# Kernel tuning notes

Measured on AMD Instinct MI355X. Metric: run time of the kernel, lower is better.

## Reference

```python
import jax, jax.numpy as jnp
import numpy as np

B, C, E, S, L, N = 2, 256, 256, 3, 5, 128
HMAX = 128
LEVEL_SIZES = np.array([128, 64, 32, 16, 8])
STRIDES = np.array([8.0, 16.0, 32.0, 64.0, 128.0])
GROUPS = 8
EPS = 1e-5


def setup_inputs() -> dict:
    key = jax.random.key(0)
    ks = jax.random.split(key, 16)
    # Padded FPN pyramid stacked as [L, B, C, HMAX, HMAX]; level l valid in [:sz, :sz]
    fm = jnp.zeros((L, B, C, HMAX, HMAX), jnp.float32)
    for l in range(L):
        sz = int(LEVEL_SIZES[l])
        fm = fm.at[l, :, :, :sz, :sz].set(jax.random.normal(ks[l], (B, C, sz, sz), jnp.float32))
    # Boxes in 1024x1024 image coordinates (x1, y1, x2, y2)
    cxy = jax.random.uniform(ks[5], (N, 2), minval=60.0, maxval=960.0)
    wh = jax.random.uniform(ks[6], (N, 2), minval=8.0, maxval=96.0)
    boxes = jnp.concatenate([cxy - wh / 2, cxy + wh / 2], axis=1)
    batch_idx = jax.random.randint(ks[7], (N,), 0, B, jnp.int32)
    level_idx = jax.random.randint(ks[8], (N,), 0, L, jnp.int32)
    sym_ids = jax.random.randint(ks[9], (N,), 0, 6, jnp.int32)
    conv_w = jax.random.normal(ks[10], (E, C, 3, 3), jnp.float32) / np.float32(np.sqrt(C * 9))
    gn_scale = jnp.ones((E,), jnp.float32)
    gn_bias = jnp.zeros((E,), jnp.float32)
    head_w = jax.random.normal(ks[11], (E, E), jnp.float32) / np.float32(np.sqrt(E))
    head_b = jnp.zeros((E,), jnp.float32)
    spat_w = jax.random.normal(ks[12], (E, 4), jnp.float32) * 0.01
    spat_b = jnp.zeros((E,), jnp.float32)
    sym_emb = jax.random.normal(ks[13], (6, E), jnp.float32) * 0.05
    fuse_w = jax.random.normal(ks[14], (6, E, E), jnp.float32) / np.float32(np.sqrt(E))
    fuse_b = jnp.zeros((6, E), jnp.float32)
    return dict(feature_maps=fm, boxes=boxes, conv_w=conv_w, gn_scale=gn_scale,
                gn_bias=gn_bias, head_w=head_w, head_b=head_b, spat_w=spat_w,
                spat_b=spat_b, sym_emb=sym_emb, fuse_w=fuse_w, fuse_b=fuse_b,
                batch_idx=batch_idx, level_idx=level_idx, sym_ids=sym_ids)


def _roi_align(fm, boxes, batch_idx, level_idx):
    # Batched roi_align (aligned=False, sampling_ratio=1) over all boxes at once.
    scale = (1.0 / jnp.asarray(STRIDES, fm.dtype))[level_idx]          # [N]
    hv = jnp.asarray(LEVEL_SIZES, fm.dtype)[level_idx]                 # [N] valid H=W per box
    x1 = boxes[:, 0] * scale; y1 = boxes[:, 1] * scale
    x2 = boxes[:, 2] * scale; y2 = boxes[:, 3] * scale
    roi_w = jnp.maximum(x2 - x1, 1.0)
    roi_h = jnp.maximum(y2 - y1, 1.0)
    off = (jnp.arange(S, dtype=fm.dtype) + 0.5) / S                    # bin centers
    xs = x1[:, None] + off[None, :] * roi_w[:, None]                   # [N,S]
    ys = y1[:, None] + off[None, :] * roi_h[:, None]                   # [N,S]
    y = jnp.broadcast_to(ys[:, :, None], (ys.shape[0], S, S))          # [N,S,S]
    x = jnp.broadcast_to(xs[:, None, :], (xs.shape[0], S, S))
    hvb = hv[:, None, None]
    valid = (y > -1.0) & (y < hvb) & (x > -1.0) & (x < hvb)
    yc = jnp.clip(y, 0.0, hvb - 1.0)
    xc = jnp.clip(x, 0.0, hvb - 1.0)
    y0 = jnp.floor(yc).astype(jnp.int32)
    x0 = jnp.floor(xc).astype(jnp.int32)
    hi = (hvb - 1.0).astype(jnp.int32)
    y1i = jnp.minimum(y0 + 1, hi)
    x1i = jnp.minimum(x0 + 1, hi)
    ly = yc - y0.astype(fm.dtype)
    lx = xc - x0.astype(fm.dtype)
    lvl = level_idx[:, None, None]
    bix = batch_idx[:, None, None]

    def g(yi, xi):
        # gather only the 4 corner pixels -> [N,S,S,C]
        return fm[lvl, bix, :, yi, xi]

    v = ((1 - ly) * (1 - lx))[..., None] * g(y0, x0) \
      + ((1 - ly) * lx)[..., None] * g(y0, x1i) \
      + (ly * (1 - lx))[..., None] * g(y1i, x0) \
      + (ly * lx)[..., None] * g(y1i, x1i)
    v = jnp.where(valid[..., None], v, 0.0)
    return jnp.transpose(v, (0, 3, 1, 2))                              # [N,C,S,S]


def _forward(feature_maps, boxes, conv_w, gn_scale, gn_bias, head_w, head_b,
             spat_w, spat_b, sym_emb, fuse_w, fuse_b, batch_idx, level_idx, sym_ids):
    roi = _roi_align(feature_maps, boxes, batch_idx, level_idx)        # [N,C,S,S]
    h = jax.lax.conv_general_dilated(roi, conv_w, (1, 1), ((1, 1), (1, 1)),
                                     dimension_numbers=('NCHW', 'OIHW', 'NCHW'))  # [N,E,S,S]
    n = h.shape[0]
    hg = h.reshape(n, GROUPS, -1)
    mu = hg.mean(-1, keepdims=True)
    var = hg.var(-1, keepdims=True)
    hg = (hg - mu) * jax.lax.rsqrt(var + EPS)
    h = hg.reshape(h.shape) * gn_scale[None, :, None, None] + gn_bias[None, :, None, None]
    h = jax.nn.relu(h)
    h = h.reshape(n, E, -1).mean(-1)                                   # spatial mean -> [N,E]
    head_out = jax.nn.relu(h @ head_w.T + head_b)                      # sym_feat_nn + ReLU
    spat = jax.nn.relu(boxes @ spat_w.T + spat_b)                      # spatial_embeddings
    fused_in = head_out + spat + sym_emb[sym_ids]                      # + class embedding
    out = jax.nn.relu(jnp.einsum('ne,nfe->nf', fused_in, fuse_w[sym_ids]) + fuse_b[sym_ids])
    return out                                                          # [N,E]


def reference(feature_maps, boxes, conv_w, gn_scale, gn_bias, head_w, head_b,
              spat_w, spat_b, sym_emb, fuse_w, fuse_b, batch_idx, level_idx, sym_ids):
    return _forward(feature_maps, boxes, conv_w, gn_scale, gn_bias, head_w, head_b,
                    spat_w, spat_b, sym_emb, fuse_w, fuse_b, batch_idx, level_idx, sym_ids)
```

## Files before the change

kernel.cpp:

```cpp
#include <hip/hip_runtime.h>
#include <hip/hip_bf16.h>


__device__ __forceinline__ float bf_lo(unsigned u) { return __uint_as_float(u << 16); }
__device__ __forceinline__ float bf_hi(unsigned u) { return __uint_as_float(u & 0xffff0000u); }
__device__ __forceinline__ unsigned short f2bf(float f) {
    __hip_bfloat16 h = __float2bfloat16(f);
    return *(unsigned short*)&h;
}

__global__ __launch_bounds__(256) void prep_k(
    const float* __restrict__ conv_w,
    const float* __restrict__ head_w, const float* __restrict__ fuse_w,
    const float* __restrict__ fm, const float* __restrict__ boxes,
    const int* __restrict__ batch_idx, const int* __restrict__ level_idx,
    unsigned short* __restrict__ w8, unsigned short* __restrict__ w9,
    float* __restrict__ head_wT, float* __restrict__ fuse_wT,
    float* __restrict__ roiT) {
    int blk = blockIdx.x;
    int t = threadIdx.x;

    if (blk < 256) {
        int c = blk, e = t;
        const float* src = conv_w + ((size_t)e * 256 + c) * 9;
        unsigned short tmp[8];
#pragma unroll
        for (int k = 0; k < 8; ++k) tmp[k] = f2bf(src[k]);
        ((uint4*)w8)[(size_t)c * 256 + e] = *(const uint4*)tmp;
        w9[(size_t)c * 256 + e] = f2bf(src[8]);
        return;
    }

    if (blk < 704) {
        __shared__ float tile[32][33];
        int q = blk - 256;
        int z = q >> 6;
        int rem = q & 63;
        int bx = (rem & 7) * 32, by = (rem >> 3) * 32;
        const float* in = (z == 0) ? head_w : fuse_w + (size_t)(z - 1) * 65536;
        float* out = (z == 0) ? head_wT : fuse_wT + (size_t)(z - 1) * 65536;
        int tx = t & 31, ty = t >> 5;
#pragma unroll
        for (int i = 0; i < 32; i += 8)
            tile[ty + i][tx] = in[(size_t)(by + ty + i) * 256 + bx + tx];
        __syncthreads();
#pragma unroll
        for (int i = 0; i < 32; i += 8)
            out[(size_t)(bx + ty + i) * 256 + by + tx] = tile[tx][ty + i];
        return;
    }

    {
        int q = blk - 704;
        int n = q / 9, p = q % 9;
        int i = p / 3, j = p % 3;
        int c = t;

        int lvl = level_idx[n];
        int b = batch_idx[n];
        const float sizes[5]  = {128.f, 64.f, 32.f, 16.f, 8.f};
        const float invstr[5] = {1.f/8.f, 1.f/16.f, 1.f/32.f, 1.f/64.f, 1.f/128.f};
        float scale = invstr[lvl];
        float hv = sizes[lvl];

        float x1 = boxes[n*4+0] * scale, y1 = boxes[n*4+1] * scale;
        float x2 = boxes[n*4+2] * scale, y2 = boxes[n*4+3] * scale;
        float rw = fmaxf(x2 - x1, 1.f), rh = fmaxf(y2 - y1, 1.f);
        float x = x1 + (((float)j + 0.5f) / 3.f) * rw;
        float y = y1 + (((float)i + 0.5f) / 3.f) * rh;

        bool valid = (y > -1.f) && (y < hv) && (x > -1.f) && (x < hv);
        float yc = fminf(fmaxf(y, 0.f), hv - 1.f);
        float xc = fminf(fmaxf(x, 0.f), hv - 1.f);
        int y0 = (int)floorf(yc), x0 = (int)floorf(xc);
        int hi = (int)(hv - 1.f);
        int y1i = min(y0 + 1, hi), x1i = min(x0 + 1, hi);
        float ly = yc - (float)y0, lx = xc - (float)x0;

        const float* base = fm + (((size_t)lvl * 2 + b) * 256 + c) * (128 * 128);
        float v00 = base[y0 * 128 + x0];
        float v01 = base[y0 * 128 + x1i];
        float v10 = base[y1i * 128 + x0];
        float v11 = base[y1i * 128 + x1i];
        float v = (1.f - ly) * (1.f - lx) * v00 + (1.f - ly) * lx * v01 +
                  ly * (1.f - lx) * v10 + ly * lx * v11;
        roiT[((size_t)n * 9 + p) * 256 + c] = valid ? v : 0.f;
    }
}

__global__ __launch_bounds__(512, 2) void conv_gn_pool(
    const float* __restrict__ roiT,
    const unsigned short* __restrict__ w8, const unsigned short* __restrict__ w9,
    const float* __restrict__ gn_scale, const float* __restrict__ gn_bias,
    float* __restrict__ pooled) {
    __shared__ float lds_roi[256 * 12];
    __shared__ float red[4 * 64 * 9];

    int n  = blockIdx.x >> 2;
    int eq = blockIdx.x & 3;
    int t = threadIdx.x;
    int e_loc = t & 63;
    int ch = t >> 6;
    int e = eq * 64 + e_loc;

    const float* rsrc = roiT + (size_t)n * 2304;
    for (int v = t; v < 2304; v += 512) {
        int p = v >> 8, c = v & 255;
        lds_roi[c * 12 + p] = rsrc[v];
    }
    __syncthreads();

    float acc[9];
#pragma unroll
    for (int p = 0; p < 9; ++p) acc[p] = 0.f;

    int c0 = ch * 32;
    for (int c = c0; c < c0 + 32; ++c) {
        float r[9];
#pragma unroll
        for (int jj = 0; jj < 9; ++jj) r[jj] = lds_roi[c * 12 + jj];
        uint4 wa = ((const uint4*)w8)[(size_t)c * 256 + e];
        unsigned short w9v = w9[(size_t)c * 256 + e];
        float wv[9];
        wv[0] = bf_lo(wa.x); wv[1] = bf_hi(wa.x);
        wv[2] = bf_lo(wa.y); wv[3] = bf_hi(wa.y);
        wv[4] = bf_lo(wa.z); wv[5] = bf_hi(wa.z);
        wv[6] = bf_lo(wa.w); wv[7] = bf_hi(wa.w);
        wv[8] = bf_lo((unsigned)w9v);
#pragma unroll
        for (int ky = 0; ky < 3; ++ky) {
#pragma unroll
            for (int kx = 0; kx < 3; ++kx) {
                float w = wv[ky * 3 + kx];
#pragma unroll
                for (int oy = 0; oy < 3; ++oy) {
                    int iy = oy + ky - 1;
                    if (iy < 0 || iy > 2) continue;
#pragma unroll
                    for (int ox = 0; ox < 3; ++ox) {
                        int ix = ox + kx - 1;
                        if (ix < 0 || ix > 2) continue;
                        acc[oy * 3 + ox] = fmaf(w, r[iy * 3 + ix], acc[oy * 3 + ox]);
                    }
                }
            }
        }
    }

    if (ch >= 4) {
#pragma unroll
        for (int p = 0; p < 9; ++p) red[((ch - 4) * 64 + e_loc) * 9 + p] = acc[p];
    }
    __syncthreads();
    if (ch < 4) {
#pragma unroll
        for (int p = 0; p < 9; ++p) acc[p] += red[(ch * 64 + e_loc) * 9 + p];
    }
    __syncthreads();
    if (ch >= 2 && ch < 4) {
#pragma unroll
        for (int p = 0; p < 9; ++p) red[((ch - 2) * 64 + e_loc) * 9 + p] = acc[p];
    }
    __syncthreads();
    if (ch < 2) {
#pragma unroll
        for (int p = 0; p < 9; ++p) acc[p] += red[(ch * 64 + e_loc) * 9 + p];
    }
    __syncthreads();
    if (ch == 1) {
#pragma unroll
        for (int p = 0; p < 9; ++p) red[e_loc * 9 + p] = acc[p];
    }
    __syncthreads();
    if (ch == 0) {
#pragma unroll
        for (int p = 0; p < 9; ++p) acc[p] += red[e_loc * 9 + p];

        float s = 0.f, sq = 0.f;
#pragma unroll
        for (int p = 0; p < 9; ++p) { s += acc[p]; sq += acc[p] * acc[p]; }
#pragma unroll
        for (int m = 16; m >= 1; m >>= 1) {
            s  += __shfl_xor(s, m, 64);
            sq += __shfl_xor(sq, m, 64);
        }
        float mean = s * (1.f / 288.f);
        float var = sq * (1.f / 288.f) - mean * mean;
        float rinv = rsqrtf(var + 1e-5f);
        float gs = gn_scale[e], gb = gn_bias[e];
        float ps = 0.f;
#pragma unroll
        for (int p = 0; p < 9; ++p) {
            float v = (acc[p] - mean) * rinv * gs + gb;
            ps += fmaxf(v, 0.f);
        }
        pooled[(size_t)n * 256 + e] = ps * (1.f / 9.f);
    }
}

__global__ __launch_bounds__(512) void head_fuse(
    const float* __restrict__ pooled, const float* __restrict__ boxes,
    const float* __restrict__ head_wT, const float* __restrict__ head_b,
    const float* __restrict__ spat_w, const float* __restrict__ spat_b,
    const float* __restrict__ sym_emb,
    const float* __restrict__ fuse_wT, const float* __restrict__ fuse_b,
    const int* __restrict__ sym_ids, float* __restrict__ out) {
    __shared__ float pl[256];
    __shared__ float part[512];
    __shared__ float fin[256];
    int n = blockIdx.x;
    int t = threadIdx.x;
    int e = t & 255;
    int kh = t >> 8;
    int sid = sym_ids[n];

    if (t < 256) pl[t] = pooled[(size_t)n * 256 + t];
    __syncthreads();

    {
        float acc = 0.f;
        const float* w = head_wT + (size_t)(kh * 128) * 256 + e;
        const float* p = pl + kh * 128;
#pragma unroll 8
        for (int k = 0; k < 128; ++k) acc = fmaf(p[k], w[k * 256], acc);
        part[t] = acc;
    }
    __syncthreads();
    if (t < 256) {
        float ho = fmaxf(part[t] + part[t + 256] + head_b[t], 0.f);
        float4 sw = ((const float4*)spat_w)[t];
        float b0 = boxes[n*4+0], b1 = boxes[n*4+1], b2 = boxes[n*4+2], b3 = boxes[n*4+3];
        float sp = fmaxf(spat_b[t] + b0*sw.x + b1*sw.y + b2*sw.z + b3*sw.w, 0.f);
        fin[t] = ho + sp + sym_emb[sid * 256 + t];
    }
    __syncthreads();
    {
        float o = 0.f;
        const float* w = fuse_wT + (size_t)sid * 65536 + (size_t)(kh * 128) * 256 + e;
        const float* p = fin + kh * 128;
#pragma unroll 8
        for (int k = 0; k < 128; ++k) o = fmaf(p[k], w[k * 256], o);
        part[t] = o;
    }
    __syncthreads();
    if (t < 256)
        out[(size_t)n * 256 + t] = fmaxf(part[t] + part[t + 256] + fuse_b[sid * 256 + t], 0.f);
}

extern "C" void kernel_launch(void* const* d_in, const int* in_sizes, int n_in,
                              void* d_out, int out_size, void* d_ws, size_t ws_size,
                              hipStream_t stream) {
    const float* fm      = (const float*)d_in[0];
    const float* boxes   = (const float*)d_in[1];
    const float* conv_w  = (const float*)d_in[2];
    const float* gn_s    = (const float*)d_in[3];
    const float* gn_b    = (const float*)d_in[4];
    const float* head_w  = (const float*)d_in[5];
    const float* head_b  = (const float*)d_in[6];
    const float* spat_w  = (const float*)d_in[7];
    const float* spat_b  = (const float*)d_in[8];
    const float* sym_emb = (const float*)d_in[9];
    const float* fuse_w  = (const float*)d_in[10];
    const float* fuse_b  = (const float*)d_in[11];
    const int* batch_idx = (const int*)d_in[12];
    const int* level_idx = (const int*)d_in[13];
    const int* sym_ids   = (const int*)d_in[14];
    float* outp = (float*)d_out;

    char* ws = (char*)d_ws;
    unsigned short* w8 = (unsigned short*)ws;
    unsigned short* w9 = (unsigned short*)(ws + 1048576);
    float* head_wT = (float*)(ws + 1179648);
    float* fuse_wT = (float*)(ws + 1441792);
    float* roiT    = (float*)(ws + 3014656);
    float* pooled  = (float*)(ws + 4194304);

    prep_k<<<1856, 256, 0, stream>>>(conv_w, head_w, fuse_w, fm, boxes,
                                     batch_idx, level_idx,
                                     w8, w9, head_wT, fuse_wT, roiT);
    conv_gn_pool<<<512, 512, 0, stream>>>(roiT, w8, w9, gn_s, gn_b, pooled);
    head_fuse<<<128, 512, 0, stream>>>(pooled, boxes, head_wT, head_b, spat_w, spat_b,
                                       sym_emb, fuse_wT, fuse_b, sym_ids, outp);
}
```

Before: 261.9 us.

## Process two ROIs per conv block to reuse weight loads, drop LDS staging

Each conv_gn_pool block now computes two boxes at once, so every bf16 weight fetch is used for two accumulator sets, and the grid is halved. The ROI values are read straight from global memory with wave-uniform addresses instead of being staged through LDS first. The wave index is made scalar with readfirstlane, and the last reduction step is split so two waves finish the two boxes in parallel. In exchange the block holds twice the accumulator registers, and there are half as many blocks to spread across the GPU.

After: 257.9 us. About the same (-1.5%).

```diff
diff --git a/kernel.cpp b/kernel.cpp
--- a/kernel.cpp
+++ b/kernel.cpp
@@ -93,40 +93,40 @@
     const unsigned short* __restrict__ w8, const unsigned short* __restrict__ w9,
     const float* __restrict__ gn_scale, const float* __restrict__ gn_bias,
     float* __restrict__ pooled) {
-    __shared__ float lds_roi[256 * 12];
-    __shared__ float red[4 * 64 * 9];
-
-    int n  = blockIdx.x >> 2;
+    __shared__ float redA[4 * 64 * 9];
+    __shared__ float redB[4 * 64 * 9];
+
+    int np = blockIdx.x >> 2;
     int eq = blockIdx.x & 3;
+    int n0 = np * 2, n1 = n0 + 1;
     int t = threadIdx.x;
     int e_loc = t & 63;
-    int ch = t >> 6;
+    int ch = __builtin_amdgcn_readfirstlane(t >> 6);
     int e = eq * 64 + e_loc;
 
-    const float* rsrc = roiT + (size_t)n * 2304;
-    for (int v = t; v < 2304; v += 512) {
-        int p = v >> 8, c = v & 255;
-        lds_roi[c * 12 + p] = rsrc[v];
-    }
-    __syncthreads();
-
-    float acc[9];
-#pragma unroll
-    for (int p = 0; p < 9; ++p) acc[p] = 0.f;
+    const float* r0 = roiT + (size_t)n0 * 2304;
+    const float* r1 = roiT + (size_t)n1 * 2304;
+
+    float acc0[9], acc1[9];
+#pragma unroll
+    for (int p = 0; p < 9; ++p) { acc0[p] = 0.f; acc1[p] = 0.f; }
 
     int c0 = ch * 32;
+#pragma unroll 4
     for (int c = c0; c < c0 + 32; ++c) {
-        float r[9];
-#pragma unroll
-        for (int jj = 0; jj < 9; ++jj) r[jj] = lds_roi[c * 12 + jj];
-        uint4 wa = ((const uint4*)w8)[(size_t)c * 256 + e];
-        unsigned short w9v = w9[(size_t)c * 256 + e];
+        float ra[9], rb[9];
+#pragma unroll
+        for (int jj = 0; jj < 9; ++jj) {
+            ra[jj] = r0[jj * 256 + c];
+            rb[jj] = r1[jj * 256 + c];
+        }
+        uint4 wa4 = ((const uint4*)w8)[(size_t)c * 256 + e];
         float wv[9];
-        wv[0] = bf_lo(wa.x); wv[1] = bf_hi(wa.x);
-        wv[2] = bf_lo(wa.y); wv[3] = bf_hi(wa.y);
-        wv[4] = bf_lo(wa.z); wv[5] = bf_hi(wa.z);
-        wv[6] = bf_lo(wa.w); wv[7] = bf_hi(wa.w);
-        wv[8] = bf_lo((unsigned)w9v);
+        wv[0] = bf_lo(wa4.x); wv[1] = bf_hi(wa4.x);
+        wv[2] = bf_lo(wa4.y); wv[3] = bf_hi(wa4.y);
+        wv[4] = bf_lo(wa4.z); wv[5] = bf_hi(wa4.z);
+        wv[6] = bf_lo(wa4.w); wv[7] = bf_hi(wa4.w);
+        wv[8] = bf_lo((unsigned)w9[(size_t)c * 256 + e]);
 #pragma unroll
         for (int ky = 0; ky < 3; ++ky) {
 #pragma unroll
@@ -140,7 +140,9 @@
                     for (int ox = 0; ox < 3; ++ox) {
                         int ix = ox + kx - 1;
                         if (ix < 0 || ix > 2) continue;
-                        acc[oy * 3 + ox] = fmaf(w, r[iy * 3 + ix], acc[oy * 3 + ox]);
+                        int o = oy * 3 + ox, in = iy * 3 + ix;
+                        acc0[o] = fmaf(w, ra[in], acc0[o]);
+                        acc1[o] = fmaf(w, rb[in], acc1[o]);
                     }
                 }
             }
@@ -149,32 +151,58 @@
 
     if (ch >= 4) {
 #pragma unroll
-        for (int p = 0; p < 9; ++p) red[((ch - 4) * 64 + e_loc) * 9 + p] = acc[p];
+        for (int p = 0; p < 9; ++p) {
+            redA[((ch - 4) * 64 + e_loc) * 9 + p] = acc0[p];
+            redB[((ch - 4) * 64 + e_loc) * 9 + p] = acc1[p];
+        }
     }
     __syncthreads();
     if (ch < 4) {
 #pragma unroll
-        for (int p = 0; p < 9; ++p) acc[p] += red[(ch * 64 + e_loc) * 9 + p];
+        for (int p = 0; p < 9; ++p) {
+            acc0[p] += redA[(ch * 64 + e_loc) * 9 + p];
+            acc1[p] += redB[(ch * 64 + e_loc) * 9 + p];
+        }
     }
     __syncthreads();
     if (ch >= 2 && ch < 4) {
 #pragma unroll
-        for (int p = 0; p < 9; ++p) red[((ch - 2) * 64 + e_loc) * 9 + p] = acc[p];
+        for (int p = 0; p < 9; ++p) {
+            redA[((ch - 2) * 64 + e_loc) * 9 + p] = acc0[p];
+            redB[((ch - 2) * 64 + e_loc) * 9 + p] = acc1[p];
+        }
     }
     __syncthreads();
     if (ch < 2) {
 #pragma unroll
-        for (int p = 0; p < 9; ++p) acc[p] += red[(ch * 64 + e_loc) * 9 + p];
+        for (int p = 0; p < 9; ++p) {
+            acc0[p] += redA[(ch * 64 + e_loc) * 9 + p];
+            acc1[p] += redB[(ch * 64 + e_loc) * 9 + p];
+        }
     }
     __syncthreads();
     if (ch == 1) {
 #pragma unroll
-        for (int p = 0; p < 9; ++p) red[e_loc * 9 + p] = acc[p];
-    }
-    __syncthreads();
+        for (int p = 0; p < 9; ++p) redA[e_loc * 9 + p] = acc0[p];
+    }
     if (ch == 0) {
 #pragma unroll
-        for (int p = 0; p < 9; ++p) acc[p] += red[e_loc * 9 + p];
+        for (int p = 0; p < 9; ++p) redB[e_loc * 9 + p] = acc1[p];
+    }
+    __syncthreads();
+
+    if (ch < 2) {
+        float acc[9];
+        int n_out;
+        if (ch == 0) {
+            n_out = n0;
+#pragma unroll
+            for (int p = 0; p < 9; ++p) acc[p] = acc0[p] + redA[e_loc * 9 + p];
+        } else {
+            n_out = n1;
+#pragma unroll
+            for (int p = 0; p < 9; ++p) acc[p] = acc1[p] + redB[e_loc * 9 + p];
+        }
 
         float s = 0.f, sq = 0.f;
 #pragma unroll
@@ -194,7 +222,7 @@
             float v = (acc[p] - mean) * rinv * gs + gb;
             ps += fmaxf(v, 0.f);
         }
-        pooled[(size_t)n * 256 + e] = ps * (1.f / 9.f);
+        pooled[(size_t)n_out * 256 + e] = ps * (1.f / 9.f);
     }
 }
 
@@ -278,7 +306,7 @@
     prep_k<<<1856, 256, 0, stream>>>(conv_w, head_w, fuse_w, fm, boxes,
                                      batch_idx, level_idx,
                                      w8, w9, head_wT, fuse_wT, roiT);
-    conv_gn_pool<<<512, 512, 0, stream>>>(roiT, w8, w9, gn_s, gn_b, pooled);
+    conv_gn_pool<<<256, 512, 0, stream>>>(roiT, w8, w9, gn_s, gn_b, pooled);
     head_fuse<<<128, 512, 0, stream>>>(pooled, boxes, head_wT, head_b, spat_w, spat_b,
                                        sym_emb, fuse_wT, fuse_b, sym_ids, outp);
 }
```
